# Kernel tuning notes

Measured on AMD Instinct MI355X. Metric: run time of the kernel, lower is better.

The kernel has to match this reference:

```python
import jax, jax.numpy as jnp
import numpy as np

C = 1.0  # curvature
EPS = 1e-5

@jax.custom_vjp
def arsinh(x):
    return jnp.log(jnp.maximum(x + jnp.sqrt(1.0 + x * x), 1e-5))

def _arsinh_fwd(x):
    return arsinh(x), x

def _arsinh_bwd(x, g):
    return (g / jnp.sqrt(1.0 + x * x),)

arsinh.defvjp(_arsinh_fwd, _arsinh_bwd)

def tanh_clamped(x, clamp=15.0):
    return jnp.tanh(jnp.clip(x, -clamp, clamp))

def expmap0(u, c):
    sqrt_c = c ** 0.5
    u_norm = jnp.maximum(jnp.linalg.norm(u, axis=-1, keepdims=True), 1e-5)
    return tanh_clamped(sqrt_c * u_norm) * u / (sqrt_c * u_norm)

def mobius_addition_batch(x, y, c):
    # x: [K, D], y: [N, D] -> [K, N, D]
    xy = jnp.einsum('kd,nd->kn', x, y)
    x2 = jnp.sum(x * x, axis=-1, keepdims=True)          # [K, 1]
    y2 = jnp.sum(y * y, axis=-1, keepdims=True)          # [N, 1]
    num = (1.0 + 2.0 * c * xy + c * y2.T)[:, :, None] * x[:, None, :]
    num = num + (1.0 - c * x2)[:, :, None] * y[None, :, :]
    denom = 1.0 + 2.0 * c * xy + (c ** 2) * x2 * y2.T    # [K, N]
    return num / (denom[:, :, None] + EPS)

def hyperbolic_softmax(x, a, p, c):
    # x: [N, D], a/p: [K, D] -> logits [N, K]
    lambda_pkc = 2.0 / (1.0 - c * jnp.minimum(jnp.sum(p * p, axis=1), 1.0 / c - 1e-4))
    k = lambda_pkc * jnp.maximum(jnp.linalg.norm(a, axis=1), 1e-7) / jnp.sqrt(c)
    mob_add = mobius_addition_batch(-p, x, c)            # [K, N, D]
    num = 2.0 * jnp.sqrt(c) * jnp.sum(mob_add * a[:, None, :], axis=-1)   # [K, N]
    denom = jnp.maximum(jnp.linalg.norm(a, axis=1, keepdims=True), 1e-7) * \
        (1.0 - c * jnp.sum(mob_add * mob_add, axis=2))   # [K, N]
    logit = k[:, None] * arsinh(num / denom)
    return logit.T                                        # [N, K]

def setup_inputs() -> dict:
    key = jax.random.key(0)
    k1, k2, k3 = jax.random.split(key, 3)
    N, K, D = 2048, 256, 512
    bound = 1.0 / np.sqrt(D)  # kaiming_uniform(a=sqrt(5)) bound
    x = jax.random.normal(k1, (N, D), dtype=jnp.float32) * 0.02  # inside unit ball
    a_vals = jax.random.uniform(k2, (K, D), dtype=jnp.float32, minval=-bound, maxval=bound)
    p_vals = jax.random.uniform(k3, (K, D), dtype=jnp.float32, minval=-bound, maxval=bound)
    return {"x": x, "a_vals": a_vals, "p_vals": p_vals}

def reference(x, a_vals, p_vals):
    c = jnp.asarray(C, dtype=x.dtype)
    p_poincare = expmap0(p_vals, c)                      # [K, D]
    conformal = 1.0 - c * jnp.sum(p_poincare * p_poincare, axis=1, keepdims=True)
    a_poincare = a_vals * conformal                      # [K, D]
    return hyperbolic_softmax(x, a_poincare, p_poincare, c)
```

## Files before the change

### kernel.cpp

```cpp
#include <hip/hip_runtime.h>
#include <hip/hip_bf16.h>
#include <math.h>

#define NROWS 2048
#define KROWS 256
#define DDIM  512

typedef __attribute__((ext_vector_type(8))) short short8;
typedef __attribute__((ext_vector_type(4))) float f32x4;

#define AB_BYTE   262144
#define SC_FOFF   131072
#define Y2_FOFF   132096
#define XB_BYTE   536576
#define WS_NEEDED (536576 + 2097152)

__device__ inline unsigned short f2bf(float f) {
    unsigned u = __float_as_uint(f);
    u += 0x7fffu + ((u >> 16) & 1u);
    return (unsigned short)(u >> 16);
}

__device__ inline float wave_reduce_sum(float v) {
    #pragma unroll
    for (int off = 32; off > 0; off >>= 1)
        v += __shfl_xor(v, off, 64);
    return v;
}

template <bool XBWS>
__global__ __launch_bounds__(256) void hmlr_prep(
        const float* __restrict__ x,
        const float* __restrict__ a_vals,
        const float* __restrict__ p_vals,
        float* __restrict__ ws) {
    const int tid  = threadIdx.x;
    const int w    = tid >> 6;
    const int lane = tid & 63;
    const int bid  = blockIdx.x;

    if (bid < 64) {
        const int k = bid * 4 + w;
        const float4* pv4 = (const float4*)(p_vals) + k * (DDIM / 4) + lane * 2;
        const float4* av4 = (const float4*)(a_vals) + k * (DDIM / 4) + lane * 2;
        float4 p0 = pv4[0], p1 = pv4[1];
        float4 a0 = av4[0], a1 = av4[1];

        float pn2 = p0.x*p0.x + p0.y*p0.y + p0.z*p0.z + p0.w*p0.w
                  + p1.x*p1.x + p1.y*p1.y + p1.z*p1.z + p1.w*p1.w;
        float an2 = a0.x*a0.x + a0.y*a0.y + a0.z*a0.z + a0.w*a0.w
                  + a1.x*a1.x + a1.y*a1.y + a1.z*a1.z + a1.w*a1.w;
        float pa0 = p0.x*a0.x + p0.y*a0.y + p0.z*a0.z + p0.w*a0.w
                  + p1.x*a1.x + p1.y*a1.y + p1.z*a1.z + p1.w*a1.w;

        pn2 = wave_reduce_sum(pn2);
        an2 = wave_reduce_sum(an2);
        pa0 = wave_reduce_sum(pa0);

        float u     = fmaxf(sqrtf(pn2), 1e-5f);
        float t     = tanhf(fminf(u, 15.0f));
        float scale = t / u;
        float p2    = scale * scale * pn2;
        float conf  = 1.0f - p2;
        float na    = fmaxf(conf * sqrtf(an2), 1e-7f);
        float pa    = scale * conf * pa0;
        float lam   = 2.0f / (1.0f - fminf(p2, 0.9999f));
        float kc    = lam * na;

        float pf[8] = { scale*p0.x, scale*p0.y, scale*p0.z, scale*p0.w,
                        scale*p1.x, scale*p1.y, scale*p1.z, scale*p1.w };
        float af[8] = { conf*a0.x, conf*a0.y, conf*a0.z, conf*a0.w,
                        conf*a1.x, conf*a1.y, conf*a1.z, conf*a1.w };
        short8 pu, au;
        #pragma unroll
        for (int j = 0; j < 8; ++j) {
            pu[j] = (short)f2bf(pf[j]);
            au[j] = (short)f2bf(af[j]);
        }
        short8* PT8 = (short8*)ws;
        short8* AT8 = (short8*)((char*)ws + AB_BYTE);
        const int ci = (((k >> 4) * 16 + (lane >> 2)) * 64) + (lane & 3) * 16 + (k & 15);
        PT8[ci] = pu;
        AT8[ci] = au;
        if (lane == 0)
            ((float4*)(ws + SC_FOFF))[k] = make_float4(p2, pa, na, kc);
    } else {
        const int row = (bid - 64) * 4 + w;
        const float4* xv4 = (const float4*)(x) + row * (DDIM / 4) + lane * 2;
        float4 x0 = xv4[0], x1 = xv4[1];
        float s = x0.x*x0.x + x0.y*x0.y + x0.z*x0.z + x0.w*x0.w
                + x1.x*x1.x + x1.y*x1.y + x1.z*x1.z + x1.w*x1.w;
        s = wave_reduce_sum(s);
        if (lane == 0) ws[Y2_FOFF + row] = s;
        if (XBWS) {
            short8* XT8 = (short8*)((char*)ws + XB_BYTE);
            short8 xu;
            xu[0] = (short)f2bf(x0.x); xu[1] = (short)f2bf(x0.y);
            xu[2] = (short)f2bf(x0.z); xu[3] = (short)f2bf(x0.w);
            xu[4] = (short)f2bf(x1.x); xu[5] = (short)f2bf(x1.y);
            xu[6] = (short)f2bf(x1.z); xu[7] = (short)f2bf(x1.w);
            const int ci = (((row >> 4) * 16 + (lane >> 2)) * 64) + (lane & 3) * 16 + (row & 15);
            XT8[ci] = xu;
        }
    }
}

template <bool XBWS>
__global__ __launch_bounds__(256, 2) void hmlr_mfma16(
        const float* __restrict__ x,
        const float* __restrict__ ws,
        float* __restrict__ out) {
    const int lane = threadIdx.x & 63;
    const int w    = threadIdx.x >> 6;
    const int mt   = blockIdx.x >> 2;
    const int ct   = (blockIdx.x & 3) * 4 + w;
    const int m0   = mt * 16;
    const int c0   = ct * 16;
    const int row  = lane & 15;
    const int kg   = lane >> 4;

    const short8* PT8 = (const short8*)ws;
    const short8* AT8 = (const short8*)((const char*)ws + AB_BYTE);
    const float* SC = ws + SC_FOFF;
    const float* Y2 = ws + Y2_FOFF;

    const short8* pt = PT8 + ct * 16 * 64 + lane;
    const short8* at = AT8 + ct * 16 * 64 + lane;

    short8 xv[16], pv[16], av[16];
    if (XBWS) {
        const short8* xt = (const short8*)((const char*)ws + XB_BYTE) + mt * 16 * 64 + lane;
        #pragma unroll
        for (int s = 0; s < 16; ++s) xv[s] = xt[s * 64];
    } else {
        const float* xr = x + (m0 + row) * DDIM + kg * 8;
        #pragma unroll
        for (int s = 0; s < 16; ++s) {
            float4 v0 = *(const float4*)(xr + s * 32);
            float4 v1 = *(const float4*)(xr + s * 32 + 4);
            short8 xu;
            xu[0] = (short)f2bf(v0.x); xu[1] = (short)f2bf(v0.y);
            xu[2] = (short)f2bf(v0.z); xu[3] = (short)f2bf(v0.w);
            xu[4] = (short)f2bf(v1.x); xu[5] = (short)f2bf(v1.y);
            xu[6] = (short)f2bf(v1.z); xu[7] = (short)f2bf(v1.w);
            xv[s] = xu;
        }
    }
    #pragma unroll
    for (int s = 0; s < 16; ++s) pv[s] = pt[s * 64];
    #pragma unroll
    for (int s = 0; s < 16; ++s) av[s] = at[s * 64];

    f32x4 aP[2] = {{0.f,0.f,0.f,0.f},{0.f,0.f,0.f,0.f}};
    f32x4 aA[2] = {{0.f,0.f,0.f,0.f},{0.f,0.f,0.f,0.f}};
    #pragma unroll
    for (int s = 0; s < 16; ++s) {
        aP[s & 1] = __builtin_amdgcn_mfma_f32_16x16x32_bf16(xv[s], pv[s], aP[s & 1], 0, 0, 0);
        aA[s & 1] = __builtin_amdgcn_mfma_f32_16x16x32_bf16(xv[s], av[s], aA[s & 1], 0, 0, 0);
    }
    f32x4 accP = aP[0] + aP[1];
    f32x4 accA = aA[0] + aA[1];

    const int c = c0 + row;
    f32x4 sc = *(const f32x4*)(SC + 4 * c);
    const float p2 = sc[0], pa = sc[1], na = sc[2], kc = sc[3];
    #pragma unroll
    for (int j = 0; j < 4; ++j) {
        const int m = m0 + kg * 4 + j;
        const float y2n = Y2[m];
        const float xpv = accP[j];
        const float xav = accA[j];
        const float alpha = 1.0f - 2.0f * xpv + y2n;
        const float beta  = 1.0f - p2;
        const float gam   = 1.0f - 2.0f * xpv + p2 * y2n;
        const float gi    = 1.0f / (gam + 1e-5f);
        const float num   = 2.0f * (beta * xav - alpha * pa) * gi;
        const float mob2  = (alpha*alpha*p2 + beta*beta*y2n
                             - 2.0f*alpha*beta*xpv) * gi * gi;
        const float den   = na * (1.0f - mob2);
        const float z     = num / den;
        out[m * KROWS + c] = kc * logf(fmaxf(z + sqrtf(1.0f + z * z), 1e-5f));
    }
}

extern "C" void kernel_launch(void* const* d_in, const int* in_sizes, int n_in,
                              void* d_out, int out_size, void* d_ws, size_t ws_size,
                              hipStream_t stream) {
    (void)in_sizes; (void)n_in; (void)out_size;
    const float* x      = (const float*)d_in[0];
    const float* a_vals = (const float*)d_in[1];
    const float* p_vals = (const float*)d_in[2];
    float* ws  = (float*)d_ws;
    float* out = (float*)d_out;

    if (ws_size >= (size_t)WS_NEEDED) {
        hmlr_prep<true><<<576, 256, 0, stream>>>(x, a_vals, p_vals, ws);
        hmlr_mfma16<true><<<512, 256, 0, stream>>>(x, ws, out);
    } else {
        hmlr_prep<false><<<576, 256, 0, stream>>>(x, a_vals, p_vals, ws);
        hmlr_mfma16<false><<<512, 256, 0, stream>>>(x, ws, out);
    }
}
```

Before: 15.94 us.

## Fuse x norm and bf16 conversion into main MFMA kernel, shrink prep

The prep kernel now handles only the K parameter rows, and drops the x row norms and the bf16 pre-conversion of x through workspace. The main kernel loads fp32 x directly, converts it to bf16 in registers, computes the row squared norms with shuffles, and broadcasts them with __shfl. Block mapping is also changed so the four waves of a block share a column tile of P/A and cover different row tiles. This removes the workspace round trip for x and most of the prep grid, at the cost of more conversion work in the main kernel, where x rows are reconverted once for each of the 16 column tiles.

```diff
diff --git a/kernel.cpp b/kernel.cpp
--- a/kernel.cpp
+++ b/kernel.cpp
@@ -11,9 +11,6 @@
 
 #define AB_BYTE   262144
 #define SC_FOFF   131072
-#define Y2_FOFF   132096
-#define XB_BYTE   536576
-#define WS_NEEDED (536576 + 2097152)
 
 __device__ inline unsigned short f2bf(float f) {
     unsigned u = __float_as_uint(f);
@@ -28,92 +25,68 @@
     return v;
 }
 
-template <bool XBWS>
 __global__ __launch_bounds__(256) void hmlr_prep(
-        const float* __restrict__ x,
         const float* __restrict__ a_vals,
         const float* __restrict__ p_vals,
         float* __restrict__ ws) {
     const int tid  = threadIdx.x;
     const int w    = tid >> 6;
     const int lane = tid & 63;
-    const int bid  = blockIdx.x;
+    const int k    = blockIdx.x * 4 + w;
 
-    if (bid < 64) {
-        const int k = bid * 4 + w;
-        const float4* pv4 = (const float4*)(p_vals) + k * (DDIM / 4) + lane * 2;
-        const float4* av4 = (const float4*)(a_vals) + k * (DDIM / 4) + lane * 2;
-        float4 p0 = pv4[0], p1 = pv4[1];
-        float4 a0 = av4[0], a1 = av4[1];
+    const float4* pv4 = (const float4*)(p_vals) + k * (DDIM / 4) + lane * 2;
+    const float4* av4 = (const float4*)(a_vals) + k * (DDIM / 4) + lane * 2;
+    float4 p0 = pv4[0], p1 = pv4[1];
+    float4 a0 = av4[0], a1 = av4[1];
 
-        float pn2 = p0.x*p0.x + p0.y*p0.y + p0.z*p0.z + p0.w*p0.w
-                  + p1.x*p1.x + p1.y*p1.y + p1.z*p1.z + p1.w*p1.w;
-        float an2 = a0.x*a0.x + a0.y*a0.y + a0.z*a0.z + a0.w*a0.w
-                  + a1.x*a1.x + a1.y*a1.y + a1.z*a1.z + a1.w*a1.w;
-        float pa0 = p0.x*a0.x + p0.y*a0.y + p0.z*a0.z + p0.w*a0.w
-                  + p1.x*a1.x + p1.y*a1.y + p1.z*a1.z + p1.w*a1.w;
+    float pn2 = p0.x*p0.x + p0.y*p0.y + p0.z*p0.z + p0.w*p0.w
+              + p1.x*p1.x + p1.y*p1.y + p1.z*p1.z + p1.w*p1.w;
+    float an2 = a0.x*a0.x + a0.y*a0.y + a0.z*a0.z + a0.w*a0.w
+              + a1.x*a1.x + a1.y*a1.y + a1.z*a1.z + a1.w*a1.w;
+    float pa0 = p0.x*a0.x + p0.y*a0.y + p0.z*a0.z + p0.w*a0.w
+              + p1.x*a1.x + p1.y*a1.y + p1.z*a1.z + p1.w*a1.w;
 
-        pn2 = wave_reduce_sum(pn2);
-        an2 = wave_reduce_sum(an2);
-        pa0 = wave_reduce_sum(pa0);
+    pn2 = wave_reduce_sum(pn2);
+    an2 = wave_reduce_sum(an2);
+    pa0 = wave_reduce_sum(pa0);
 
-        float u     = fmaxf(sqrtf(pn2), 1e-5f);
-        float t     = tanhf(fminf(u, 15.0f));
-        float scale = t / u;
-        float p2    = scale * scale * pn2;
-        float conf  = 1.0f - p2;
-        float na    = fmaxf(conf * sqrtf(an2), 1e-7f);
-        float pa    = scale * conf * pa0;
-        float lam   = 2.0f / (1.0f - fminf(p2, 0.9999f));
-        float kc    = lam * na;
+    float u     = fmaxf(sqrtf(pn2), 1e-5f);
+    float t     = tanhf(fminf(u, 15.0f));
+    float scale = t / u;
+    float p2    = scale * scale * pn2;
+    float conf  = 1.0f - p2;
+    float na    = fmaxf(conf * sqrtf(an2), 1e-7f);
+    float pa    = scale * conf * pa0;
+    float lam   = 2.0f / (1.0f - fminf(p2, 0.9999f));
+    float kc    = lam * na;
 
-        float pf[8] = { scale*p0.x, scale*p0.y, scale*p0.z, scale*p0.w,
-                        scale*p1.x, scale*p1.y, scale*p1.z, scale*p1.w };
-        float af[8] = { conf*a0.x, conf*a0.y, conf*a0.z, conf*a0.w,
-                        conf*a1.x, conf*a1.y, conf*a1.z, conf*a1.w };
-        short8 pu, au;
-        #pragma unroll
-        for (int j = 0; j < 8; ++j) {
-            pu[j] = (short)f2bf(pf[j]);
-            au[j] = (short)f2bf(af[j]);
-        }
-        short8* PT8 = (short8*)ws;
-        short8* AT8 = (short8*)((char*)ws + AB_BYTE);
-        const int ci = (((k >> 4) * 16 + (lane >> 2)) * 64) + (lane & 3) * 16 + (k & 15);
-        PT8[ci] = pu;
-        AT8[ci] = au;
-        if (lane == 0)
-            ((float4*)(ws + SC_FOFF))[k] = make_float4(p2, pa, na, kc);
-    } else {
-        const int row = (bid - 64) * 4 + w;
-        const float4* xv4 = (const float4*)(x) + row * (DDIM / 4) + lane * 2;
-        float4 x0 = xv4[0], x1 = xv4[1];
-        float s = x0.x*x0.x + x0.y*x0.y + x0.z*x0.z + x0.w*x0.w
-                + x1.x*x1.x + x1.y*x1.y + x1.z*x1.z + x1.w*x1.w;
-        s = wave_reduce_sum(s);
-        if (lane == 0) ws[Y2_FOFF + row] = s;
-        if (XBWS) {
-            short8* XT8 = (short8*)((char*)ws + XB_BYTE);
-            short8 xu;
-            xu[0] = (short)f2bf(x0.x); xu[1] = (short)f2bf(x0.y);
-            xu[2] = (short)f2bf(x0.z); xu[3] = (short)f2bf(x0.w);
-            xu[4] = (short)f2bf(x1.x); xu[5] = (short)f2bf(x1.y);
-            xu[6] = (short)f2bf(x1.z); xu[7] = (short)f2bf(x1.w);
-            const int ci = (((row >> 4) * 16 + (lane >> 2)) * 64) + (lane & 3) * 16 + (row & 15);
-            XT8[ci] = xu;
-        }
+    float pf[8] = { scale*p0.x, scale*p0.y, scale*p0.z, scale*p0.w,
+                    scale*p1.x, scale*p1.y, scale*p1.z, scale*p1.w };
+    float af[8] = { conf*a0.x, conf*a0.y, conf*a0.z, conf*a0.w,
+                    conf*a1.x, conf*a1.y, conf*a1.z, conf*a1.w };
+    short8 pu, au;
+    #pragma unroll
+    for (int j = 0; j < 8; ++j) {
+        pu[j] = (short)f2bf(pf[j]);
+        au[j] = (short)f2bf(af[j]);
     }
+    short8* PT8 = (short8*)ws;
+    short8* AT8 = (short8*)((char*)ws + AB_BYTE);
+    const int ci = (((k >> 4) * 16 + (lane >> 2)) * 64) + (lane & 3) * 16 + (k & 15);
+    PT8[ci] = pu;
+    AT8[ci] = au;
+    if (lane == 0)
+        ((float4*)(ws + SC_FOFF))[k] = make_float4(p2, pa, na, kc);
 }
 
-template <bool XBWS>
-__global__ __launch_bounds__(256, 2) void hmlr_mfma16(
+__global__ __launch_bounds__(256, 2) void hmlr_main(
         const float* __restrict__ x,
         const float* __restrict__ ws,
         float* __restrict__ out) {
     const int lane = threadIdx.x & 63;
     const int w    = threadIdx.x >> 6;
-    const int mt   = blockIdx.x >> 2;
-    const int ct   = (blockIdx.x & 3) * 4 + w;
+    const int ct   = blockIdx.x & 15;
+    const int mt   = (blockIdx.x >> 4) * 4 + w;
     const int m0   = mt * 16;
     const int c0   = ct * 16;
     const int row  = lane & 15;
@@ -121,31 +94,31 @@
 
     const short8* PT8 = (const short8*)ws;
     const short8* AT8 = (const short8*)((const char*)ws + AB_BYTE);
-    const float* SC = ws + SC_FOFF;
-    const float* Y2 = ws + Y2_FOFF;
+    const float*  SC  = ws + SC_FOFF;
 
     const short8* pt = PT8 + ct * 16 * 64 + lane;
     const short8* at = AT8 + ct * 16 * 64 + lane;
 
-    short8 xv[16], pv[16], av[16];
-    if (XBWS) {
-        const short8* xt = (const short8*)((const char*)ws + XB_BYTE) + mt * 16 * 64 + lane;
-        #pragma unroll
-        for (int s = 0; s < 16; ++s) xv[s] = xt[s * 64];
-    } else {
-        const float* xr = x + (m0 + row) * DDIM + kg * 8;
-        #pragma unroll
-        for (int s = 0; s < 16; ++s) {
-            float4 v0 = *(const float4*)(xr + s * 32);
-            float4 v1 = *(const float4*)(xr + s * 32 + 4);
-            short8 xu;
-            xu[0] = (short)f2bf(v0.x); xu[1] = (short)f2bf(v0.y);
-            xu[2] = (short)f2bf(v0.z); xu[3] = (short)f2bf(v0.w);
-            xu[4] = (short)f2bf(v1.x); xu[5] = (short)f2bf(v1.y);
-            xu[6] = (short)f2bf(v1.z); xu[7] = (short)f2bf(v1.w);
-            xv[s] = xu;
-        }
+    short8 xv[16];
+    float  ss = 0.0f;
+    const float* xr = x + (m0 + row) * DDIM + kg * 8;
+    #pragma unroll
+    for (int s = 0; s < 16; ++s) {
+        float4 v0 = *(const float4*)(xr + s * 32);
+        float4 v1 = *(const float4*)(xr + s * 32 + 4);
+        ss += v0.x*v0.x + v0.y*v0.y + v0.z*v0.z + v0.w*v0.w
+            + v1.x*v1.x + v1.y*v1.y + v1.z*v1.z + v1.w*v1.w;
+        short8 xu;
+        xu[0] = (short)f2bf(v0.x); xu[1] = (short)f2bf(v0.y);
+        xu[2] = (short)f2bf(v0.z); xu[3] = (short)f2bf(v0.w);
+        xu[4] = (short)f2bf(v1.x); xu[5] = (short)f2bf(v1.y);
+        xu[6] = (short)f2bf(v1.z); xu[7] = (short)f2bf(v1.w);
+        xv[s] = xu;
     }
+    ss += __shfl_xor(ss, 16, 64);
+    ss += __shfl_xor(ss, 32, 64);
+
+    short8 pv[16], av[16];
     #pragma unroll
     for (int s = 0; s < 16; ++s) pv[s] = pt[s * 64];
     #pragma unroll
@@ -166,8 +139,8 @@
     const float p2 = sc[0], pa = sc[1], na = sc[2], kc = sc[3];
     #pragma unroll
     for (int j = 0; j < 4; ++j) {
-        const int m = m0 + kg * 4 + j;
-        const float y2n = Y2[m];
+        const int m     = m0 + kg * 4 + j;
+        const float y2n = __shfl(ss, kg * 4 + j, 64);
         const float xpv = accP[j];
         const float xav = accA[j];
         const float alpha = 1.0f - 2.0f * xpv + y2n;
@@ -186,18 +159,13 @@
 extern "C" void kernel_launch(void* const* d_in, const int* in_sizes, int n_in,
                               void* d_out, int out_size, void* d_ws, size_t ws_size,
                               hipStream_t stream) {
-    (void)in_sizes; (void)n_in; (void)out_size;
+    (void)in_sizes; (void)n_in; (void)out_size; (void)ws_size;
     const float* x      = (const float*)d_in[0];
     const float* a_vals = (const float*)d_in[1];
     const float* p_vals = (const float*)d_in[2];
     float* ws  = (float*)d_ws;
     float* out = (float*)d_out;
 
-    if (ws_size >= (size_t)WS_NEEDED) {
-        hmlr_prep<true><<<576, 256, 0, stream>>>(x, a_vals, p_vals, ws);
-        hmlr_mfma16<true><<<512, 256, 0, stream>>>(x, ws, out);
-    } else {
-        hmlr_prep<false><<<576, 256, 0, stream>>>(x, a_vals, p_vals, ws);
-        hmlr_mfma16<false><<<512, 256, 0, stream>>>(x, ws, out);
-    }
+    hmlr_prep<<<64, 256, 0, stream>>>(a_vals, p_vals, ws);
+    hmlr_main<<<512, 256, 0, stream>>>(x, ws, out);
 }
```

After: 21.86 us. +37.2%, slower.

## Split reduction dimension across wave pairs and use fast-math intrinsics in epilogue

Applied to the files above, without the earlier changes.

The main kernel now has each pair of waves split the D=512 reduction in half, exchanging partial MFMA accumulators through shared memory. Each wave then computes half of the epilogue rows. The grid doubles to 1024 blocks with a higher occupancy hint, which shortens each wave's serial MFMA chain and register footprint. The epilogue swaps exact divide, sqrt and log for hardware rcp, sqrt and __logf approximations, which adds some precision risk. In the no-workspace path, x norms are now computed inside the main kernel so the prep kernel launches only the p/a blocks; that path is inactive by default.

```diff
diff --git a/kernel.cpp b/kernel.cpp
--- a/kernel.cpp
+++ b/kernel.cpp
@@ -106,14 +106,20 @@
 }
 
 template <bool XBWS>
-__global__ __launch_bounds__(256, 2) void hmlr_mfma16(
+__global__ __launch_bounds__(256, 4) void hmlr_main_split(
         const float* __restrict__ x,
         const float* __restrict__ ws,
         float* __restrict__ out) {
+    __shared__ f32x4 ex[4][2][64];
+    __shared__ float exs[4][64];
+
     const int lane = threadIdx.x & 63;
     const int w    = threadIdx.x >> 6;
-    const int mt   = blockIdx.x >> 2;
-    const int ct   = (blockIdx.x & 3) * 4 + w;
+    const int ci   = w >> 1;
+    const int h    = w & 1;
+    const int mt   = blockIdx.x >> 3;
+    const int cp   = blockIdx.x & 7;
+    const int ct   = cp * 2 + ci;
     const int m0   = mt * 16;
     const int c0   = ct * 16;
     const int row  = lane & 15;
@@ -121,23 +127,27 @@
 
     const short8* PT8 = (const short8*)ws;
     const short8* AT8 = (const short8*)((const char*)ws + AB_BYTE);
-    const float* SC = ws + SC_FOFF;
-    const float* Y2 = ws + Y2_FOFF;
-
-    const short8* pt = PT8 + ct * 16 * 64 + lane;
-    const short8* at = AT8 + ct * 16 * 64 + lane;
-
-    short8 xv[16], pv[16], av[16];
+    const float*  SC  = ws + SC_FOFF;
+    const float*  Y2  = ws + Y2_FOFF;
+
+    const short8* pt = PT8 + ct * 16 * 64 + h * 8 * 64 + lane;
+    const short8* at = AT8 + ct * 16 * 64 + h * 8 * 64 + lane;
+
+    short8 xv[8];
+    float  ss = 0.0f;
     if (XBWS) {
-        const short8* xt = (const short8*)((const char*)ws + XB_BYTE) + mt * 16 * 64 + lane;
+        const short8* xt = (const short8*)((const char*)ws + XB_BYTE)
+                           + mt * 16 * 64 + h * 8 * 64 + lane;
         #pragma unroll
-        for (int s = 0; s < 16; ++s) xv[s] = xt[s * 64];
+        for (int s = 0; s < 8; ++s) xv[s] = xt[s * 64];
     } else {
-        const float* xr = x + (m0 + row) * DDIM + kg * 8;
+        const float* xr = x + (m0 + row) * DDIM + h * 256 + kg * 8;
         #pragma unroll
-        for (int s = 0; s < 16; ++s) {
+        for (int s = 0; s < 8; ++s) {
             float4 v0 = *(const float4*)(xr + s * 32);
             float4 v1 = *(const float4*)(xr + s * 32 + 4);
+            ss += v0.x*v0.x + v0.y*v0.y + v0.z*v0.z + v0.w*v0.w
+                + v1.x*v1.x + v1.y*v1.y + v1.z*v1.z + v1.w*v1.w;
             short8 xu;
             xu[0] = (short)f2bf(v0.x); xu[1] = (short)f2bf(v0.y);
             xu[2] = (short)f2bf(v0.z); xu[3] = (short)f2bf(v0.w);
@@ -145,41 +155,55 @@
             xu[6] = (short)f2bf(v1.z); xu[7] = (short)f2bf(v1.w);
             xv[s] = xu;
         }
-    }
-    #pragma unroll
-    for (int s = 0; s < 16; ++s) pv[s] = pt[s * 64];
-    #pragma unroll
-    for (int s = 0; s < 16; ++s) av[s] = at[s * 64];
+        ss += __shfl_xor(ss, 16, 64);
+        ss += __shfl_xor(ss, 32, 64);
+    }
+    short8 pv[8], av[8];
+    #pragma unroll
+    for (int s = 0; s < 8; ++s) pv[s] = pt[s * 64];
+    #pragma unroll
+    for (int s = 0; s < 8; ++s) av[s] = at[s * 64];
 
     f32x4 aP[2] = {{0.f,0.f,0.f,0.f},{0.f,0.f,0.f,0.f}};
     f32x4 aA[2] = {{0.f,0.f,0.f,0.f},{0.f,0.f,0.f,0.f}};
     #pragma unroll
-    for (int s = 0; s < 16; ++s) {
+    for (int s = 0; s < 8; ++s) {
         aP[s & 1] = __builtin_amdgcn_mfma_f32_16x16x32_bf16(xv[s], pv[s], aP[s & 1], 0, 0, 0);
         aA[s & 1] = __builtin_amdgcn_mfma_f32_16x16x32_bf16(xv[s], av[s], aA[s & 1], 0, 0, 0);
     }
     f32x4 accP = aP[0] + aP[1];
     f32x4 accA = aA[0] + aA[1];
+
+    ex[w][0][lane] = accP;
+    ex[w][1][lane] = accA;
+    if (!XBWS) exs[w][lane] = ss;
+    __syncthreads();
+    const int pw = w ^ 1;
+    accP += ex[pw][0][lane];
+    accA += ex[pw][1][lane];
+    float ssf = XBWS ? 0.0f : (ss + exs[pw][lane]);
 
     const int c = c0 + row;
     f32x4 sc = *(const f32x4*)(SC + 4 * c);
     const float p2 = sc[0], pa = sc[1], na = sc[2], kc = sc[3];
     #pragma unroll
-    for (int j = 0; j < 4; ++j) {
-        const int m = m0 + kg * 4 + j;
-        const float y2n = Y2[m];
+    for (int jj = 0; jj < 2; ++jj) {
+        const int j     = 2 * h + jj;
+        const int m     = m0 + kg * 4 + j;
+        const float y2n = XBWS ? Y2[m] : __shfl(ssf, kg * 4 + j, 64);
         const float xpv = accP[j];
         const float xav = accA[j];
         const float alpha = 1.0f - 2.0f * xpv + y2n;
         const float beta  = 1.0f - p2;
         const float gam   = 1.0f - 2.0f * xpv + p2 * y2n;
-        const float gi    = 1.0f / (gam + 1e-5f);
+        const float gi    = __builtin_amdgcn_rcpf(gam + 1e-5f);
         const float num   = 2.0f * (beta * xav - alpha * pa) * gi;
         const float mob2  = (alpha*alpha*p2 + beta*beta*y2n
                              - 2.0f*alpha*beta*xpv) * gi * gi;
         const float den   = na * (1.0f - mob2);
-        const float z     = num / den;
-        out[m * KROWS + c] = kc * logf(fmaxf(z + sqrtf(1.0f + z * z), 1e-5f));
+        const float z     = num * __builtin_amdgcn_rcpf(den);
+        const float arg   = fmaxf(z + __builtin_amdgcn_sqrtf(1.0f + z * z), 1e-5f);
+        out[m * KROWS + c] = kc * __logf(arg);
     }
 }
 
@@ -195,9 +219,9 @@
 
     if (ws_size >= (size_t)WS_NEEDED) {
         hmlr_prep<true><<<576, 256, 0, stream>>>(x, a_vals, p_vals, ws);
-        hmlr_mfma16<true><<<512, 256, 0, stream>>>(x, ws, out);
+        hmlr_main_split<true><<<1024, 256, 0, stream>>>(x, ws, out);
     } else {
-        hmlr_prep<false><<<576, 256, 0, stream>>>(x, a_vals, p_vals, ws);
-        hmlr_mfma16<false><<<512, 256, 0, stream>>>(x, ws, out);
-    }
-}
+        hmlr_prep<false><<<64, 256, 0, stream>>>(x, a_vals, p_vals, ws);
+        hmlr_main_split<false><<<1024, 256, 0, stream>>>(x, ws, out);
+    }
+}
```

New measurement: 16.14 us. Within noise of the previous version (+1.3%).
